# Kernel tuning notes

Measured on AMD Instinct MI355X. Metric: run time of the kernel, lower is better.

Reference implementation:

```python
import jax, jax.numpy as jnp
import numpy as np

N_NODES = 10000
IN_CH = 128
HID = 256
OUT_CH = 1
N_EDGES_ADJ = 320000  # avg degree 32
N_TARGET = 8192


def setup_inputs() -> dict:
    key = jax.random.key(0)
    ks = jax.random.split(key, 16)
    s = 0.05  # weight scale for numerical stability
    inp = {
        'x': jax.random.normal(ks[0], (N_NODES, IN_CH), jnp.float32),
        'adj_row': jax.random.randint(ks[1], (N_EDGES_ADJ,), 0, N_NODES),
        'adj_col': jax.random.randint(ks[2], (N_EDGES_ADJ,), 0, N_NODES),
        'tar_ei': jax.random.randint(ks[3], (2, N_TARGET), 0, N_NODES),
        'beta': jnp.ones((1,), jnp.float32),
        'W1': s * jax.random.normal(ks[4], (IN_CH, HID), jnp.float32),
        'b1': jnp.zeros((HID,), jnp.float32),
        'W2': s * jax.random.normal(ks[5], (HID, HID), jnp.float32),
        'b2': jnp.zeros((HID,), jnp.float32),
        'W3': s * jax.random.normal(ks[6], (HID, HID), jnp.float32),
        'b3': jnp.zeros((HID,), jnp.float32),
        'Wij1': s * jax.random.normal(ks[7], (IN_CH, HID), jnp.float32),
        'bij1': jnp.zeros((HID,), jnp.float32),
        'Wij2': s * jax.random.normal(ks[8], (HID, HID), jnp.float32),
        'bij2': jnp.zeros((HID,), jnp.float32),
        'Wl1': s * jax.random.normal(ks[9], (HID, HID), jnp.float32),
        'bl1': jnp.zeros((HID,), jnp.float32),
        'Wl2': s * jax.random.normal(ks[10], (HID, OUT_CH), jnp.float32),
        'bl2': jnp.zeros((OUT_CH,), jnp.float32),
    }
    return inp


def reference(x, adj_row, adj_col, tar_ei, beta, W1, b1, W2, b2, W3, b3,
              Wij1, bij1, Wij2, bij2, Wl1, bl1, Wl2, bl2):
    n = x.shape[0]
    # Binary adjacency (duplicates collapse to 1, matching SparseTensor semantics)
    A = jnp.zeros((n, n), x.dtype).at[adj_row, adj_col].set(1.0)
    xi = x[tar_ei[0]]  # [E, F]
    xj = x[tar_ei[1]]  # [E, F]
    # adjoverlap: common-neighbor indicator per target edge, then spmm_add with x
    cn_mask = A[tar_ei[0]] * A[tar_ei[1]]          # [E, N]
    cn_x = cn_mask @ x                              # [E, F] sum of features over common neighbors
    # xcnlin: Linear-ReLU-Linear-ReLU-Linear (eval mode: dropout=identity, ln=identity)
    xcn = jax.nn.relu(cn_x @ W1 + b1)
    xcn = jax.nn.relu(xcn @ W2 + b2)
    xcn = xcn @ W3 + b3
    # xijlin: Linear-ReLU-Linear
    xij = jax.nn.relu((xi * xj) @ Wij1 + bij1) @ Wij2 + bij2
    # lin head: Linear-ReLU-Linear
    h = jax.nn.relu((xcn * beta + xij) @ Wl1 + bl1)
    return h @ Wl2 + bl2  # [E, 1]
```

## Files before the change

kernel.cpp:

```cpp
#include <hip/hip_runtime.h>
#include <hip/hip_bf16.h>

#define N_NODES 10000
#define IN_CH 128
#define HID 256
#define E_TAR 8192
#define N_EDGES 320000
#define WPR 320
#define WUSED 313
#define MASK_WORDS (N_NODES * WPR)
#define CSR_MAX 128
#define BM 32

typedef short bf16x8 __attribute__((ext_vector_type(8)));
typedef short bf16x4 __attribute__((ext_vector_type(4)));
typedef float f32x4 __attribute__((ext_vector_type(4)));

__device__ __forceinline__ unsigned short f2bf(float f) {
  union { float f; unsigned u; } v; v.f = f;
  unsigned r = v.u + 0x7fffu + ((v.u >> 16) & 1u);
  return (unsigned short)(r >> 16);
}
__device__ __forceinline__ float bf2f(unsigned short h) {
  union { unsigned u; float f; } v; v.u = ((unsigned)h) << 16; return v.f;
}

__global__ void fill_zero(uint4* __restrict__ p, int n4) {
  int i = blockIdx.x * 256 + threadIdx.x;
  int stride = gridDim.x * 256;
  uint4 z = {0u, 0u, 0u, 0u};
  for (; i < n4; i += stride) p[i] = z;
}

__global__ void scatter_adj(const int* __restrict__ row, const int* __restrict__ col,
                            unsigned* __restrict__ mask) {
  int k = blockIdx.x * 256 + threadIdx.x;
  if (k < N_EDGES) {
    int r = row[k], c = col[k];
    atomicOr(&mask[(size_t)r * WPR + (c >> 5)], 1u << (c & 31));
  }
}

__global__ void csr_build(const unsigned* __restrict__ mask, int* __restrict__ deg,
                          int* __restrict__ csr) {
  int row = blockIdx.x * 4 + (threadIdx.x >> 6);
  int lane = threadIdx.x & 63;
  const unsigned* mr = mask + (size_t)row * WPR;
  unsigned words[5];
  int cnt = 0;
  #pragma unroll
  for (int t = 0; t < 5; ++t) {
    int w = lane + 64 * t;
    unsigned v = (w < WUSED) ? mr[w] : 0u;
    words[t] = v;
    cnt += __popc(v);
  }
  int pre = cnt;
  #pragma unroll
  for (int off = 1; off < 64; off <<= 1) {
    int n2 = __shfl_up(pre, off);
    if (lane >= off) pre += n2;
  }
  int excl = pre - cnt;
  int total = __shfl(pre, 63);
  if (lane == 0) deg[row] = total;
  int p = excl;
  int* dst = csr + (size_t)row * CSR_MAX;
  #pragma unroll
  for (int t = 0; t < 5; ++t) {
    unsigned v = words[t];
    int wbase = (lane + 64 * t) * 32;
    while (v) {
      int b = __ffs(v) - 1;
      v &= v - 1;
      if (p < CSR_MAX) dst[p] = wbase + b;
      ++p;
    }
  }
}

__global__ void cn_gather_csr(const unsigned* __restrict__ mask, const int* __restrict__ deg,
                              const int* __restrict__ csr, const int* __restrict__ tar,
                              const float* __restrict__ x, float* __restrict__ cnx) {
  __shared__ int lists[4][256];
  __shared__ int cnts[4];
  int wv = threadIdx.x >> 6, lane = threadIdx.x & 63;
  int e = blockIdx.x * 4 + wv;
  int i = tar[e], j = tar[E_TAR + e];
  int di = deg[i], dj = deg[j];
  int a = (di <= dj) ? i : j;
  int b = (di <= dj) ? j : i;
  int da = min(di, dj);
  if (lane == 0) cnts[wv] = 0;
  __syncthreads();
  const unsigned* mb = mask + (size_t)b * WPR;
  if (da <= CSR_MAX) {
    const int* la = csr + (size_t)a * CSR_MAX;
    for (int t = lane; t < da; t += 64) {
      int n = la[t];
      if ((mb[n >> 5] >> (n & 31)) & 1u) {
        int p = atomicAdd(&cnts[wv], 1);
        lists[wv][p] = n;
      }
    }
  } else {
    const unsigned* ma = mask + (size_t)a * WPR;
    for (int w = lane; w < WUSED; w += 64) {
      unsigned v = ma[w] & mb[w];
      while (v) {
        int bit = __ffs(v) - 1;
        v &= v - 1;
        int p = atomicAdd(&cnts[wv], 1);
        if (p < 256) lists[wv][p] = w * 32 + bit;
      }
    }
  }
  __syncthreads();
  int n = cnts[wv]; if (n > 256) n = 256;
  float a0 = 0.f, a1 = 0.f;
  for (int t = 0; t < n; ++t) {
    const float* xr = x + (size_t)lists[wv][t] * IN_CH;
    a0 += xr[lane];
    a1 += xr[lane + 64];
  }
  cnx[(size_t)e * IN_CH + lane] = a0;
  cnx[(size_t)e * IN_CH + 64 + lane] = a1;
}

__global__ void prep_w(const float* W1, const float* W2, const float* W3,
                       const float* Wij1, const float* Wij2, const float* Wl1,
                       unsigned short* wts) {
  int bid = blockIdx.x;
  const float* W; unsigned short* O; int K, t;
  if      (bid <  32) { W = W1;   O = wts;          K = 128; t = bid; }
  else if (bid <  96) { W = W2;   O = wts + 32768;  K = 256; t = bid - 32; }
  else if (bid < 160) { W = W3;   O = wts + 98304;  K = 256; t = bid - 96; }
  else if (bid < 192) { W = Wij1; O = wts + 163840; K = 128; t = bid - 160; }
  else if (bid < 256) { W = Wij2; O = wts + 196608; K = 256; t = bid - 192; }
  else                { W = Wl1;  O = wts + 262144; K = 256; t = bid - 256; }
  const int N = 256;
  int tpk = K / 32;
  int tk = t % tpk, tn = t / tpk;
  __shared__ float tile[32][33];
  int tid = threadIdx.x;
  int c = tid & 31, r0 = tid >> 5;
  #pragma unroll
  for (int rr = 0; rr < 32; rr += 8)
    tile[r0 + rr][c] = W[(size_t)(tk * 32 + r0 + rr) * N + tn * 32 + c];
  __syncthreads();
  #pragma unroll
  for (int rr = 0; rr < 32; rr += 8)
    O[(size_t)(tn * 32 + r0 + rr) * K + tk * 32 + c] = f2bf(tile[c][r0 + rr]);
}

template<int K>
__device__ __forceinline__ void gemm_core(const unsigned short (*A)[264],
                                          const unsigned short* __restrict__ Wt,
                                          int lane, int wm, int wn, f32x4* acc) {
  int l15 = lane & 15, kg = (lane >> 4) * 8;
  const unsigned short* wb = Wt + (size_t)(wn + l15) * K + kg;
  bf16x8 bc[4], bn_[4];
  #pragma unroll
  for (int f = 0; f < 4; ++f) bc[f] = *(const bf16x8*)(wb + f * 16 * K);
  #pragma unroll
  for (int k0 = 0; k0 < K; k0 += 32) {
    bf16x8 a = *(const bf16x8*)&A[wm + l15][k0 + kg];
    if (k0 + 32 < K) {
      #pragma unroll
      for (int f = 0; f < 4; ++f) bn_[f] = *(const bf16x8*)(wb + f * 16 * K + k0 + 32);
    }
    #pragma unroll
    for (int f = 0; f < 4; ++f)
      acc[f] = __builtin_amdgcn_mfma_f32_16x16x32_bf16(a, bc[f], acc[f], 0, 0, 0);
    #pragma unroll
    for (int f = 0; f < 4; ++f) bc[f] = bn_[f];
  }
}

__device__ __forceinline__ void epi_store(unsigned short (*dst)[264], f32x4* acc,
                                          const float* __restrict__ bias, bool relu,
                                          int lane, int wm, int wn) {
  int l15 = lane & 15, rq = (lane >> 4) * 4;
  #pragma unroll
  for (int f = 0; f < 4; ++f) {
    float bv = bias[wn + f * 16 + l15];
    #pragma unroll
    for (int i = 0; i < 4; ++i) {
      float v = acc[f][i] + bv;
      if (relu) v = fmaxf(v, 0.f);
      dst[wm + rq + i][wn + f * 16 + l15] = f2bf(v);
    }
  }
}

__global__ __launch_bounds__(512) void fused_mlp(
    const float* __restrict__ cn_x, const float* __restrict__ x, const int* __restrict__ tar,
    const unsigned short* __restrict__ wts,
    const float* __restrict__ b1, const float* __restrict__ b2, const float* __restrict__ b3,
    const float* __restrict__ bij1, const float* __restrict__ bij2, const float* __restrict__ bl1,
    const float* __restrict__ Wl2, const float* __restrict__ bl2,
    const float* __restrict__ betaPtr, float* __restrict__ out)
{
  __shared__ unsigned short P[BM][264];
  __shared__ unsigned short Q[BM][264];
  const unsigned short* Wt1   = wts;
  const unsigned short* Wt2   = wts + 32768;
  const unsigned short* Wt3   = wts + 98304;
  const unsigned short* Wtij1 = wts + 163840;
  const unsigned short* Wtij2 = wts + 196608;
  const unsigned short* Wtl1  = wts + 262144;

  int m0 = blockIdx.x * BM;
  int tid = threadIdx.x;
  int lane = tid & 63, wv = tid >> 6;
  int wm = (wv >> 2) * 16;
  int wn = (wv & 3) * 64;
  float beta_v = betaPtr[0];

  {
    int row = tid >> 4, seg = tid & 15;
    const float* src = cn_x + (size_t)(m0 + row) * IN_CH + seg * 8;
    f32x4 u0 = *(const f32x4*)src, u1 = *(const f32x4*)(src + 4);
    unsigned short tmp[8];
    #pragma unroll
    for (int u = 0; u < 4; ++u) { tmp[u] = f2bf(u0[u]); tmp[4 + u] = f2bf(u1[u]); }
    *(bf16x8*)&P[row][seg * 8] = *(bf16x8*)tmp;
  }
  __syncthreads();

  f32x4 acc[4];
  #pragma unroll
  for (int f = 0; f < 4; ++f) acc[f] = (f32x4){0.f, 0.f, 0.f, 0.f};
  gemm_core<128>(P, Wt1, lane, wm, wn, acc);
  epi_store(Q, acc, b1, true, lane, wm, wn);
  __syncthreads();

  #pragma unroll
  for (int f = 0; f < 4; ++f) acc[f] = (f32x4){0.f, 0.f, 0.f, 0.f};
  gemm_core<256>(Q, Wt2, lane, wm, wn, acc);
  epi_store(P, acc, b2, true, lane, wm, wn);
  __syncthreads();

  f32x4 xcn[4];
  #pragma unroll
  for (int f = 0; f < 4; ++f) xcn[f] = (f32x4){0.f, 0.f, 0.f, 0.f};
  gemm_core<256>(P, Wt3, lane, wm, wn, xcn);
  {
    int l15 = lane & 15;
    #pragma unroll
    for (int f = 0; f < 4; ++f) {
      float bv = b3[wn + f * 16 + l15];
      #pragma unroll
      for (int i = 0; i < 4; ++i) xcn[f][i] += bv;
    }
  }
  __syncthreads();

  {
    int row = tid >> 4, seg = tid & 15;
    int gi = tar[m0 + row], gj = tar[E_TAR + m0 + row];
    const float* xi = x + (size_t)gi * IN_CH + seg * 8;
    const float* xj = x + (size_t)gj * IN_CH + seg * 8;
    f32x4 i0 = *(const f32x4*)xi, i1 = *(const f32x4*)(xi + 4);
    f32x4 j0 = *(const f32x4*)xj, j1 = *(const f32x4*)(xj + 4);
    unsigned short tmp[8];
    #pragma unroll
    for (int u = 0; u < 4; ++u) {
      tmp[u] = f2bf(i0[u] * j0[u]);
      tmp[4 + u] = f2bf(i1[u] * j1[u]);
    }
    *(bf16x8*)&P[row][seg * 8] = *(bf16x8*)tmp;
  }
  __syncthreads();

  #pragma unroll
  for (int f = 0; f < 4; ++f) acc[f] = (f32x4){0.f, 0.f, 0.f, 0.f};
  gemm_core<128>(P, Wtij1, lane, wm, wn, acc);
  epi_store(Q, acc, bij1, true, lane, wm, wn);
  __syncthreads();

  #pragma unroll
  for (int f = 0; f < 4; ++f) acc[f] = (f32x4){0.f, 0.f, 0.f, 0.f};
  gemm_core<256>(Q, Wtij2, lane, wm, wn, acc);
  {
    int l15 = lane & 15, rq = (lane >> 4) * 4;
    #pragma unroll
    for (int f = 0; f < 4; ++f) {
      float bv = bij2[wn + f * 16 + l15];
      #pragma unroll
      for (int i = 0; i < 4; ++i) {
        float v = acc[f][i] + bv + beta_v * xcn[f][i];
        P[wm + rq + i][wn + f * 16 + l15] = f2bf(v);
      }
    }
  }
  __syncthreads();

  #pragma unroll
  for (int f = 0; f < 4; ++f) acc[f] = (f32x4){0.f, 0.f, 0.f, 0.f};
  gemm_core<256>(P, Wtl1, lane, wm, wn, acc);
  epi_store(Q, acc, bl1, true, lane, wm, wn);
  __syncthreads();

  {
    f32x4 w2v = *(const f32x4*)&Wl2[lane * 4];
    float bl2v = bl2[0];
    #pragma unroll
    for (int rr = 0; rr < 4; ++rr) {
      int r = wv * 4 + rr;
      bf16x4 q = *(const bf16x4*)&Q[r][lane * 4];
      float s = 0.f;
      #pragma unroll
      for (int u = 0; u < 4; ++u) s += bf2f((unsigned short)q[u]) * w2v[u];
      #pragma unroll
      for (int off = 32; off; off >>= 1) s += __shfl_down(s, off);
      if (lane == 0) out[m0 + r] = s + bl2v;
    }
  }
}

extern "C" void kernel_launch(void* const* d_in, const int* in_sizes, int n_in,
                              void* d_out, int out_size, void* d_ws, size_t ws_size,
                              hipStream_t stream) {
  const float* x      = (const float*)d_in[0];
  const int*   adj_r  = (const int*)d_in[1];
  const int*   adj_c  = (const int*)d_in[2];
  const int*   tar    = (const int*)d_in[3];
  const float* beta   = (const float*)d_in[4];
  const float* W1     = (const float*)d_in[5];
  const float* b1     = (const float*)d_in[6];
  const float* W2     = (const float*)d_in[7];
  const float* b2     = (const float*)d_in[8];
  const float* W3     = (const float*)d_in[9];
  const float* b3     = (const float*)d_in[10];
  const float* Wij1   = (const float*)d_in[11];
  const float* bij1   = (const float*)d_in[12];
  const float* Wij2   = (const float*)d_in[13];
  const float* bij2   = (const float*)d_in[14];
  const float* Wl1    = (const float*)d_in[15];
  const float* bl1    = (const float*)d_in[16];
  const float* Wl2    = (const float*)d_in[17];
  const float* bl2    = (const float*)d_in[18];

  char* ws = (char*)d_ws;
  unsigned*       mask = (unsigned*)ws;
  int*            deg  = (int*)(ws + (size_t)14 * 1024 * 1024);
  int*            csr  = (int*)(ws + (size_t)15 * 1024 * 1024);
  float*          cnx  = (float*)(ws + (size_t)21 * 1024 * 1024);
  unsigned short* wts  = (unsigned short*)(ws + (size_t)26 * 1024 * 1024);

  prep_w<<<320, 256, 0, stream>>>(W1, W2, W3, Wij1, Wij2, Wl1, wts);
  fill_zero<<<3200, 256, 0, stream>>>((uint4*)mask, MASK_WORDS / 4);
  scatter_adj<<<(N_EDGES + 255) / 256, 256, 0, stream>>>(adj_r, adj_c, mask);
  csr_build<<<N_NODES / 4, 256, 0, stream>>>(mask, deg, csr);
  cn_gather_csr<<<E_TAR / 4, 256, 0, stream>>>(mask, deg, csr, tar, x, cnx);
  fused_mlp<<<E_TAR / BM, 512, 0, stream>>>(cnx, x, tar, wts,
                                            b1, b2, b3, bij1, bij2, bl1,
                                            Wl2, bl2, beta, (float*)d_out);
}
```

Baseline: 82.76 us.

## Build CSR during atomic scatter and restructure MLP warp tiling with register-held weights

Removes the separate csr_build kernel: scatter_adj now uses the atomicOr return value to detect new bits, then appends the column to a per-row CSR list with an atomicAdd on deg (deg is zeroed together with the mask). CSR lists become unordered. The fused MLP is remapped so each of the 8 waves covers all 32 rows and 32 columns. Each wave preloads the next layer's full weight slice into registers, overlapping those loads with the current layer's epilogue, and hoists the biases and x gathers to the kernel start. This trades extra register pressure (launch_bounds 512,2) and more LDS A-reads for fewer weight-fetch stalls and one less launch.

```diff
diff --git a/kernel.cpp b/kernel.cpp
--- a/kernel.cpp
+++ b/kernel.cpp
@@ -33,48 +33,16 @@
 }
 
 __global__ void scatter_adj(const int* __restrict__ row, const int* __restrict__ col,
-                            unsigned* __restrict__ mask) {
+                            unsigned* __restrict__ mask, int* __restrict__ deg,
+                            int* __restrict__ csr) {
   int k = blockIdx.x * 256 + threadIdx.x;
   if (k < N_EDGES) {
     int r = row[k], c = col[k];
-    atomicOr(&mask[(size_t)r * WPR + (c >> 5)], 1u << (c & 31));
-  }
-}
-
-__global__ void csr_build(const unsigned* __restrict__ mask, int* __restrict__ deg,
-                          int* __restrict__ csr) {
-  int row = blockIdx.x * 4 + (threadIdx.x >> 6);
-  int lane = threadIdx.x & 63;
-  const unsigned* mr = mask + (size_t)row * WPR;
-  unsigned words[5];
-  int cnt = 0;
-  #pragma unroll
-  for (int t = 0; t < 5; ++t) {
-    int w = lane + 64 * t;
-    unsigned v = (w < WUSED) ? mr[w] : 0u;
-    words[t] = v;
-    cnt += __popc(v);
-  }
-  int pre = cnt;
-  #pragma unroll
-  for (int off = 1; off < 64; off <<= 1) {
-    int n2 = __shfl_up(pre, off);
-    if (lane >= off) pre += n2;
-  }
-  int excl = pre - cnt;
-  int total = __shfl(pre, 63);
-  if (lane == 0) deg[row] = total;
-  int p = excl;
-  int* dst = csr + (size_t)row * CSR_MAX;
-  #pragma unroll
-  for (int t = 0; t < 5; ++t) {
-    unsigned v = words[t];
-    int wbase = (lane + 64 * t) * 32;
-    while (v) {
-      int b = __ffs(v) - 1;
-      v &= v - 1;
-      if (p < CSR_MAX) dst[p] = wbase + b;
-      ++p;
+    unsigned bit = 1u << (c & 31);
+    unsigned old = atomicOr(&mask[(size_t)r * WPR + (c >> 5)], bit);
+    if (!(old & bit)) {
+      int p = atomicAdd(&deg[r], 1);
+      if (p < CSR_MAX) csr[(size_t)r * CSR_MAX + p] = c;
     }
   }
 }
@@ -153,47 +121,35 @@
     O[(size_t)(tn * 32 + r0 + rr) * K + tk * 32 + c] = f2bf(tile[c][r0 + rr]);
 }
 
+template<int KN>
+__device__ __forceinline__ void loadB(const unsigned short* __restrict__ Wt,
+                                      int wn, int l15, int kg,
+                                      bf16x8* b0, bf16x8* b1) {
+  const unsigned short* p0 = Wt + (size_t)(wn + l15) * KN + kg;
+  const unsigned short* p1 = Wt + (size_t)(wn + 16 + l15) * KN + kg;
+  #pragma unroll
+  for (int s = 0; s < KN / 32; ++s) {
+    b0[s] = *(const bf16x8*)(p0 + s * 32);
+    b1[s] = *(const bf16x8*)(p1 + s * 32);
+  }
+}
+
 template<int K>
-__device__ __forceinline__ void gemm_core(const unsigned short (*A)[264],
-                                          const unsigned short* __restrict__ Wt,
-                                          int lane, int wm, int wn, f32x4* acc) {
-  int l15 = lane & 15, kg = (lane >> 4) * 8;
-  const unsigned short* wb = Wt + (size_t)(wn + l15) * K + kg;
-  bf16x8 bc[4], bn_[4];
-  #pragma unroll
-  for (int f = 0; f < 4; ++f) bc[f] = *(const bf16x8*)(wb + f * 16 * K);
-  #pragma unroll
-  for (int k0 = 0; k0 < K; k0 += 32) {
-    bf16x8 a = *(const bf16x8*)&A[wm + l15][k0 + kg];
-    if (k0 + 32 < K) {
-      #pragma unroll
-      for (int f = 0; f < 4; ++f) bn_[f] = *(const bf16x8*)(wb + f * 16 * K + k0 + 32);
-    }
-    #pragma unroll
-    for (int f = 0; f < 4; ++f)
-      acc[f] = __builtin_amdgcn_mfma_f32_16x16x32_bf16(a, bc[f], acc[f], 0, 0, 0);
-    #pragma unroll
-    for (int f = 0; f < 4; ++f) bc[f] = bn_[f];
-  }
-}
-
-__device__ __forceinline__ void epi_store(unsigned short (*dst)[264], f32x4* acc,
-                                          const float* __restrict__ bias, bool relu,
-                                          int lane, int wm, int wn) {
-  int l15 = lane & 15, rq = (lane >> 4) * 4;
-  #pragma unroll
-  for (int f = 0; f < 4; ++f) {
-    float bv = bias[wn + f * 16 + l15];
-    #pragma unroll
-    for (int i = 0; i < 4; ++i) {
-      float v = acc[f][i] + bv;
-      if (relu) v = fmaxf(v, 0.f);
-      dst[wm + rq + i][wn + f * 16 + l15] = f2bf(v);
-    }
-  }
-}
-
-__global__ __launch_bounds__(512) void fused_mlp(
+__device__ __forceinline__ void computeL(const unsigned short (*A)[264],
+                                         const bf16x8* b0, const bf16x8* b1,
+                                         int l15, int kg, f32x4 acc[2][2]) {
+  #pragma unroll
+  for (int s = 0; s < K / 32; ++s) {
+    bf16x8 a0 = *(const bf16x8*)&A[l15][s * 32 + kg];
+    bf16x8 a1 = *(const bf16x8*)&A[16 + l15][s * 32 + kg];
+    acc[0][0] = __builtin_amdgcn_mfma_f32_16x16x32_bf16(a0, b0[s], acc[0][0], 0, 0, 0);
+    acc[1][0] = __builtin_amdgcn_mfma_f32_16x16x32_bf16(a1, b0[s], acc[1][0], 0, 0, 0);
+    acc[0][1] = __builtin_amdgcn_mfma_f32_16x16x32_bf16(a0, b1[s], acc[0][1], 0, 0, 0);
+    acc[1][1] = __builtin_amdgcn_mfma_f32_16x16x32_bf16(a1, b1[s], acc[1][1], 0, 0, 0);
+  }
+}
+
+__global__ __launch_bounds__(512, 2) void fused_mlp(
     const float* __restrict__ cn_x, const float* __restrict__ x, const int* __restrict__ tar,
     const unsigned short* __restrict__ wts,
     const float* __restrict__ b1, const float* __restrict__ b2, const float* __restrict__ b3,
@@ -213,12 +169,28 @@
   int m0 = blockIdx.x * BM;
   int tid = threadIdx.x;
   int lane = tid & 63, wv = tid >> 6;
-  int wm = (wv >> 2) * 16;
-  int wn = (wv & 3) * 64;
+  int wn = wv * 32;
+  int l15 = lane & 15, kg = (lane >> 4) * 8, rq = (lane >> 4) * 4;
+
+  bf16x8 B0[8], B1[8];
+  loadB<128>(Wt1, wn, l15, kg, B0, B1);
+
+  int row = tid >> 4, seg = tid & 15;
+  int gi = tar[m0 + row], gj = tar[E_TAR + m0 + row];
+  const float* xip = x + (size_t)gi * IN_CH + seg * 8;
+  const float* xjp = x + (size_t)gj * IN_CH + seg * 8;
+  f32x4 xi0 = *(const f32x4*)xip, xi1 = *(const f32x4*)(xip + 4);
+  f32x4 xj0 = *(const f32x4*)xjp, xj1 = *(const f32x4*)(xjp + 4);
+  float bv1[2]   = { b1[wn + l15],   b1[wn + 16 + l15] };
+  float bv2[2]   = { b2[wn + l15],   b2[wn + 16 + l15] };
+  float bv3[2]   = { b3[wn + l15],   b3[wn + 16 + l15] };
+  float bvij1[2] = { bij1[wn + l15], bij1[wn + 16 + l15] };
+  float bvij2[2] = { bij2[wn + l15], bij2[wn + 16 + l15] };
+  float bvl1[2]  = { bl1[wn + l15],  bl1[wn + 16 + l15] };
   float beta_v = betaPtr[0];
+  f32x4 w2v = *(const f32x4*)&Wl2[lane * 4];
 
   {
-    int row = tid >> 4, seg = tid & 15;
     const float* src = cn_x + (size_t)(m0 + row) * IN_CH + seg * 8;
     f32x4 u0 = *(const f32x4*)src, u1 = *(const f32x4*)(src + 4);
     unsigned short tmp[8];
@@ -228,82 +200,79 @@
   }
   __syncthreads();
 
-  f32x4 acc[4];
-  #pragma unroll
-  for (int f = 0; f < 4; ++f) acc[f] = (f32x4){0.f, 0.f, 0.f, 0.f};
-  gemm_core<128>(P, Wt1, lane, wm, wn, acc);
-  epi_store(Q, acc, b1, true, lane, wm, wn);
-  __syncthreads();
-
-  #pragma unroll
-  for (int f = 0; f < 4; ++f) acc[f] = (f32x4){0.f, 0.f, 0.f, 0.f};
-  gemm_core<256>(Q, Wt2, lane, wm, wn, acc);
-  epi_store(P, acc, b2, true, lane, wm, wn);
-  __syncthreads();
-
-  f32x4 xcn[4];
-  #pragma unroll
-  for (int f = 0; f < 4; ++f) xcn[f] = (f32x4){0.f, 0.f, 0.f, 0.f};
-  gemm_core<256>(P, Wt3, lane, wm, wn, xcn);
+  f32x4 acc[2][2];
+  #define ZACC { acc[0][0]=(f32x4){0,0,0,0}; acc[0][1]=(f32x4){0,0,0,0}; \
+                 acc[1][0]=(f32x4){0,0,0,0}; acc[1][1]=(f32x4){0,0,0,0}; }
+  #define EPI(dst, bv, RELU) { \
+    _Pragma("unroll") for (int nf = 0; nf < 2; ++nf) { \
+      int cg = wn + nf * 16 + l15; \
+      _Pragma("unroll") for (int m = 0; m < 2; ++m) \
+        _Pragma("unroll") for (int i = 0; i < 4; ++i) { \
+          float v = acc[m][nf][i] + bv[nf]; \
+          if (RELU) v = fmaxf(v, 0.f); \
+          dst[m * 16 + rq + i][cg] = f2bf(v); \
+        } \
+    } }
+
+  ZACC; computeL<128>(P, B0, B1, l15, kg, acc);
+  loadB<256>(Wt2, wn, l15, kg, B0, B1);
+  EPI(Q, bv1, 1);
+  __syncthreads();
+
+  ZACC; computeL<256>(Q, B0, B1, l15, kg, acc);
+  loadB<256>(Wt3, wn, l15, kg, B0, B1);
+  EPI(P, bv2, 1);
+  __syncthreads();
+
+  f32x4 xcn[2][2];
+  xcn[0][0]=(f32x4){0,0,0,0}; xcn[0][1]=(f32x4){0,0,0,0};
+  xcn[1][0]=(f32x4){0,0,0,0}; xcn[1][1]=(f32x4){0,0,0,0};
+  computeL<256>(P, B0, B1, l15, kg, xcn);
+  loadB<128>(Wtij1, wn, l15, kg, B0, B1);
+  #pragma unroll
+  for (int nf = 0; nf < 2; ++nf)
+    #pragma unroll
+    for (int m = 0; m < 2; ++m)
+      #pragma unroll
+      for (int i = 0; i < 4; ++i) xcn[m][nf][i] += bv3[nf];
+  __syncthreads();
+
   {
-    int l15 = lane & 15;
-    #pragma unroll
-    for (int f = 0; f < 4; ++f) {
-      float bv = b3[wn + f * 16 + l15];
-      #pragma unroll
-      for (int i = 0; i < 4; ++i) xcn[f][i] += bv;
-    }
-  }
-  __syncthreads();
-
-  {
-    int row = tid >> 4, seg = tid & 15;
-    int gi = tar[m0 + row], gj = tar[E_TAR + m0 + row];
-    const float* xi = x + (size_t)gi * IN_CH + seg * 8;
-    const float* xj = x + (size_t)gj * IN_CH + seg * 8;
-    f32x4 i0 = *(const f32x4*)xi, i1 = *(const f32x4*)(xi + 4);
-    f32x4 j0 = *(const f32x4*)xj, j1 = *(const f32x4*)(xj + 4);
     unsigned short tmp[8];
     #pragma unroll
     for (int u = 0; u < 4; ++u) {
-      tmp[u] = f2bf(i0[u] * j0[u]);
-      tmp[4 + u] = f2bf(i1[u] * j1[u]);
+      tmp[u] = f2bf(xi0[u] * xj0[u]);
+      tmp[4 + u] = f2bf(xi1[u] * xj1[u]);
     }
     *(bf16x8*)&P[row][seg * 8] = *(bf16x8*)tmp;
   }
   __syncthreads();
 
-  #pragma unroll
-  for (int f = 0; f < 4; ++f) acc[f] = (f32x4){0.f, 0.f, 0.f, 0.f};
-  gemm_core<128>(P, Wtij1, lane, wm, wn, acc);
-  epi_store(Q, acc, bij1, true, lane, wm, wn);
-  __syncthreads();
-
-  #pragma unroll
-  for (int f = 0; f < 4; ++f) acc[f] = (f32x4){0.f, 0.f, 0.f, 0.f};
-  gemm_core<256>(Q, Wtij2, lane, wm, wn, acc);
-  {
-    int l15 = lane & 15, rq = (lane >> 4) * 4;
-    #pragma unroll
-    for (int f = 0; f < 4; ++f) {
-      float bv = bij2[wn + f * 16 + l15];
+  ZACC; computeL<128>(P, B0, B1, l15, kg, acc);
+  loadB<256>(Wtij2, wn, l15, kg, B0, B1);
+  EPI(Q, bvij1, 1);
+  __syncthreads();
+
+  ZACC; computeL<256>(Q, B0, B1, l15, kg, acc);
+  loadB<256>(Wtl1, wn, l15, kg, B0, B1);
+  #pragma unroll
+  for (int nf = 0; nf < 2; ++nf) {
+    int cg = wn + nf * 16 + l15;
+    #pragma unroll
+    for (int m = 0; m < 2; ++m)
       #pragma unroll
       for (int i = 0; i < 4; ++i) {
-        float v = acc[f][i] + bv + beta_v * xcn[f][i];
-        P[wm + rq + i][wn + f * 16 + l15] = f2bf(v);
+        float v = acc[m][nf][i] + bvij2[nf] + beta_v * xcn[m][nf][i];
+        P[m * 16 + rq + i][cg] = f2bf(v);
       }
-    }
-  }
-  __syncthreads();
-
-  #pragma unroll
-  for (int f = 0; f < 4; ++f) acc[f] = (f32x4){0.f, 0.f, 0.f, 0.f};
-  gemm_core<256>(P, Wtl1, lane, wm, wn, acc);
-  epi_store(Q, acc, bl1, true, lane, wm, wn);
+  }
+  __syncthreads();
+
+  ZACC; computeL<256>(P, B0, B1, l15, kg, acc);
+  EPI(Q, bvl1, 1);
   __syncthreads();
 
   {
-    f32x4 w2v = *(const f32x4*)&Wl2[lane * 4];
     float bl2v = bl2[0];
     #pragma unroll
     for (int rr = 0; rr < 4; ++rr) {
@@ -344,15 +313,14 @@
 
   char* ws = (char*)d_ws;
   unsigned*       mask = (unsigned*)ws;
-  int*            deg  = (int*)(ws + (size_t)14 * 1024 * 1024);
+  int*            deg  = (int*)(ws + (size_t)MASK_WORDS * 4);
   int*            csr  = (int*)(ws + (size_t)15 * 1024 * 1024);
   float*          cnx  = (float*)(ws + (size_t)21 * 1024 * 1024);
   unsigned short* wts  = (unsigned short*)(ws + (size_t)26 * 1024 * 1024);
 
   prep_w<<<320, 256, 0, stream>>>(W1, W2, W3, Wij1, Wij2, Wl1, wts);
-  fill_zero<<<3200, 256, 0, stream>>>((uint4*)mask, MASK_WORDS / 4);
-  scatter_adj<<<(N_EDGES + 255) / 256, 256, 0, stream>>>(adj_r, adj_c, mask);
-  csr_build<<<N_NODES / 4, 256, 0, stream>>>(mask, deg, csr);
+  fill_zero<<<3200, 256, 0, stream>>>((uint4*)mask, (MASK_WORDS + N_NODES) / 4);
+  scatter_adj<<<(N_EDGES + 255) / 256, 256, 0, stream>>>(adj_r, adj_c, mask, deg, csr);
   cn_gather_csr<<<E_TAR / 4, 256, 0, stream>>>(mask, deg, csr, tar, x, cnx);
   fused_mlp<<<E_TAR / BM, 512, 0, stream>>>(cnx, x, tar, wts,
                                             b1, b2, b3, bij1, bij2, bl1,
```

After: 77.00 us. -7.0%, faster.
